# Kernel tuning notes

Measured on AMD Instinct MI355X. Metric: run time of the kernel, lower is better.

The kernel has to match this reference:

```python
import jax, jax.numpy as jnp
import numpy as np

EPS = 1e-5
SLOPE = 0.01  # torch LeakyReLU default negative slope


def _bn(h, gamma, beta):
    # BatchNorm1d in training mode: biased batch statistics over the batch dim
    mu = jnp.mean(h, axis=0)
    var = jnp.var(h, axis=0)
    return gamma * (h - mu) * jax.lax.rsqrt(var + EPS) + beta


def _leaky(h):
    return jnp.where(h >= 0, h, SLOPE * h)


def _forward(x, adj, w_gc1, b_gc1, w_gc2, b_gc2, w_gc3, b_gc3,
             w_fc0, b_fc0, g_fc0, be_fc0, w_fc1, b_fc1, g_fc1, be_fc1, w_fc2, b_fc2):
    B, S, Fp1 = x.shape
    F = Fp1 - 1
    N = adj.shape[0]
    # --- scatter: build per-sample node features from first S-1 timesteps ---
    sids = x[:, :S - 1, -2].astype(jnp.int32)                                   # [B,S-1]
    feats = jnp.concatenate([x[:, :S - 1, :-2], x[:, :S - 1, -1:]], axis=-1)    # [B,S-1,F]
    X = jnp.zeros((B, N, F), x.dtype).at[jnp.arange(B)[:, None], sids].set(feats)
    # --- symmetric-normalized adjacency with self loops: D^-1/2 (A+I) D^-1/2 ---
    A = adj + jnp.eye(N, dtype=adj.dtype)
    d = jax.lax.rsqrt(jnp.sum(A, axis=1))
    Ahat = d[:, None] * A * d[None, :]                                          # [N,N]
    # --- fc0 branch on last-timestep features ---
    h0 = _leaky(_bn(x[:, -1, :-2] @ w_fc0 + b_fc0, g_fc0, be_fc0))              # [B,FH]
    # --- 3-layer GCN: relu(Ahat @ X @ W + b) ---
    X = jax.nn.relu(jnp.einsum('mn,bnf->bmf', Ahat, X) @ w_gc1 + b_gc1)
    X = jax.nn.relu(jnp.einsum('mn,bnf->bmf', Ahat, X) @ w_gc2 + b_gc2)
    X = jax.nn.relu(jnp.einsum('mn,bnf->bmf', Ahat, X) @ w_gc3 + b_gc3)         # [B,N,GH]
    # --- gather station-specific rows ---
    sid_last = x[:, -1, -2].astype(jnp.int32)                                   # [B]
    g = X[jnp.arange(B), sid_last]                                              # [B,GH]
    # --- fusion MLP head ---
    h = jnp.concatenate([h0, g], axis=1)
    h = _leaky(_bn(h @ w_fc1 + b_fc1, g_fc1, be_fc1))
    return jax.nn.sigmoid(h @ w_fc2 + b_fc2)                                    # [B,1]


def setup_inputs() -> dict:
    B, N, S, F = 128, 2000, 64, 16
    GH, FH = 512, 512
    key = jax.random.key(0)
    ks = jax.random.split(key, 12)
    x = jax.random.normal(ks[0], (B, S, F + 1), dtype=jnp.float32)
    # station-id column (-2): unique ids per sample so scatter writes are unambiguous
    perms = jax.vmap(lambda k: jax.random.permutation(k, N)[:S])(jax.random.split(ks[1], B))  # [B,S]
    x = x.at[:, :, -2].set(perms.astype(jnp.float32))
    # random symmetric 0/1 adjacency, avg degree ~32
    adj = (jax.random.uniform(ks[2], (N, N)) < (32.0 / N)).astype(jnp.float32)
    adj = jnp.maximum(adj, adj.T)

    def lin(k, i, o):
        kw, kb = jax.random.split(k)
        bound = 1.0 / np.sqrt(i)
        w = jax.random.uniform(kw, (i, o), jnp.float32, -bound, bound)
        b = jax.random.uniform(kb, (o,), jnp.float32, -bound, bound)
        return w, b

    w_gc1, b_gc1 = lin(ks[3], F, GH // 2)
    w_gc2, b_gc2 = lin(ks[4], GH // 2, GH // 2)
    w_gc3, b_gc3 = lin(ks[5], GH // 2, GH)
    w_fc0, b_fc0 = lin(ks[6], F - 1, FH)
    w_fc1, b_fc1 = lin(ks[7], GH + FH, FH)
    w_fc2, b_fc2 = lin(ks[8], FH, 1)
    g_fc0 = jnp.ones((FH,), jnp.float32)
    be_fc0 = jnp.zeros((FH,), jnp.float32)
    g_fc1 = jnp.ones((FH,), jnp.float32)
    be_fc1 = jnp.zeros((FH,), jnp.float32)
    return dict(x=x, adj=adj, w_gc1=w_gc1, b_gc1=b_gc1, w_gc2=w_gc2, b_gc2=b_gc2,
                w_gc3=w_gc3, b_gc3=b_gc3, w_fc0=w_fc0, b_fc0=b_fc0, g_fc0=g_fc0, be_fc0=be_fc0,
                w_fc1=w_fc1, b_fc1=b_fc1, g_fc1=g_fc1, be_fc1=be_fc1, w_fc2=w_fc2, b_fc2=b_fc2)


def reference(x, adj, w_gc1, b_gc1, w_gc2, b_gc2, w_gc3, b_gc3, w_fc0, b_fc0, g_fc0, be_fc0,
              w_fc1, b_fc1, g_fc1, be_fc1, w_fc2, b_fc2):
    return _forward(x, adj, w_gc1, b_gc1, w_gc2, b_gc2, w_gc3, b_gc3,
                    w_fc0, b_fc0, g_fc0, be_fc0, w_fc1, b_fc1, g_fc1, be_fc1, w_fc2, b_fc2)
```

## Files before the change

kernel.cpp:

```cpp
#include <hip/hip_runtime.h>
#include <hip/hip_bf16.h>

typedef __hip_bfloat16 bf16;
typedef short s8v __attribute__((ext_vector_type(8)));
typedef float f4v __attribute__((ext_vector_type(4)));
typedef float f2v __attribute__((ext_vector_type(2)));

#define B   128
#define N   2000
#define S   64
#define CAP 128
#define JT  16
#define JG  8
#define XROW 1088

__device__ inline ushort bfb(float v) {
    union { __hip_bfloat16 h; ushort u; } c; c.h = __float2bfloat16(v); return c.u;
}

__global__ __launch_bounds__(256) void k_prep0(const float* __restrict__ adj,
                                               float* __restrict__ d,
                                               const float* __restrict__ w1,
                                               const float* __restrict__ w2,
                                               uint4* __restrict__ wf1,
                                               uint4* __restrict__ wf2) {
    int blk = blockIdx.x;
    if (blk < N) {
        int m = blk;
        const float* row = adj + (size_t)m * N;
        float s = 0.f;
        for (int c = threadIdx.x; c < N; c += 256) s += row[c];
        for (int o = 32; o > 0; o >>= 1) s += __shfl_down(s, o);
        __shared__ float red[4];
        int wave = threadIdx.x >> 6;
        if ((threadIdx.x & 63) == 0) red[wave] = s;
        __syncthreads();
        if (threadIdx.x == 0)
            d[m] = rsqrtf(red[0] + red[1] + red[2] + red[3] + 1.0f);
    } else {
        int blk2 = blk - N;
        if (blk2 < 4) {
            int e = blk2 * 256 + threadIdx.x;
            int ct = e >> 6, l = e & 63;
            int kg = l >> 4, ch = ct * 16 + (l & 15);
            ushort h[8];
#pragma unroll
            for (int j = 0; j < 8; ++j) {
                int f = kg * 8 + j;
                h[j] = (f < 16) ? bfb(w1[f * 256 + ch]) : (ushort)0;
            }
            uint4 r;
            r.x = h[0] | ((uint)h[1] << 16);
            r.y = h[2] | ((uint)h[3] << 16);
            r.z = h[4] | ((uint)h[5] << 16);
            r.w = h[6] | ((uint)h[7] << 16);
            wf1[e] = r;
        } else {
            int e = (blk2 - 4) * 256 + threadIdx.x;
            int l = e & 63;
            int kc = (e >> 6) & 7;
            int nt = e >> 9;
            int col = l & 15, kg = l >> 4;
            ushort h[8];
#pragma unroll
            for (int i = 0; i < 8; ++i) {
                int k = kc * 32 + kg * 8 + i;
                h[i] = bfb(w2[k * 256 + nt * 16 + col]);
            }
            uint4 r;
            r.x = h[0] | ((uint)h[1] << 16);
            r.y = h[2] | ((uint)h[3] << 16);
            r.z = h[4] | ((uint)h[5] << 16);
            r.w = h[6] | ((uint)h[7] << 16);
            wf2[e] = r;
        }
    }
}

__global__ __launch_bounds__(256) void k_prep1(const float* __restrict__ adj,
                                               const float* __restrict__ d,
                                               const float* __restrict__ x,
                                               int* __restrict__ cnt,
                                               int* __restrict__ idx,
                                               float* __restrict__ val,
                                               int* __restrict__ sid,
                                               int* __restrict__ sid_last,
                                               uint4* __restrict__ feA,
                                               const float* __restrict__ w0,
                                               const float* __restrict__ b0,
                                               float* __restrict__ hp0,
                                               float* __restrict__ mu0,
                                               float* __restrict__ rstd0) {
    int blk = blockIdx.x;
    if (blk < 500) {
        int m = blk * 4 + (threadIdx.x >> 6);
        int lane = threadIdx.x & 63;
        const float* row = adj + (size_t)m * N;
        float dm = d[m];
        int base = 0;
        for (int c0 = 0; c0 < N; c0 += 64) {
            int c = c0 + lane;
            float a = 0.f;
            if (c < N) { a = row[c]; if (c == m) a += 1.0f; }
            bool pred = (a != 0.f);
            unsigned long long mask = __ballot(pred);
            int pos = base + __popcll(mask & ((1ull << lane) - 1ull));
            if (pred && pos < CAP) {
                idx[m * CAP + pos] = c;
                val[m * CAP + pos] = dm * d[c] * a;
            }
            base += (int)__popcll(mask);
        }
        if (lane == 0) cnt[m] = base < CAP ? base : CAP;
    } else if (blk < 500 + B) {
        int b = blk - 500, tid = threadIdx.x;
        const float* xb = x + (size_t)b * XROW;
        __shared__ float dss_sh[63];
        __shared__ float fe_sh[64][16];
        if (tid < S - 1) {
            int s_ = (int)xb[tid * 17 + 15];
            sid[b * (S - 1) + tid] = s_;
            dss_sh[tid] = d[s_];
        }
        if (tid == S - 1) sid_last[b] = (int)xb[(S - 1) * 17 + 15];
        if (tid >= 240 && tid < 256) fe_sh[63][tid - 240] = 0.f;
        __syncthreads();
        for (int i = tid; i < (S - 1) * 16; i += 256) {
            int t = i >> 4, f = i & 15;
            fe_sh[t][f] = dss_sh[t] * xb[t * 17 + (f < 15 ? f : 16)];
        }
        __syncthreads();
        if (tid < 128) {
            int kc = tid >> 6, l = tid & 63;
            int f = l & 15, tg = l >> 4;
            ushort h[8];
#pragma unroll
            for (int j = 0; j < 8; ++j)
                h[j] = bfb(fe_sh[kc * 32 + tg * 8 + j][f]);
            uint4 r;
            r.x = h[0] | ((uint)h[1] << 16);
            r.y = h[2] | ((uint)h[3] << 16);
            r.z = h[4] | ((uint)h[5] << 16);
            r.w = h[6] | ((uint)h[7] << 16);
            feA[(b * 2 + kc) * 64 + l] = r;
        }
    } else {
        int tid = threadIdx.x;
        int c = tid >> 7, b = tid & 127;
        int o = (blk - 500 - B) * 2 + c;
        const float* xr = x + (size_t)b * XROW + (S - 1) * 17;
        float acc = b0[o];
#pragma unroll
        for (int f = 0; f < 15; ++f) acc += xr[f] * w0[f * 512 + o];
        hp0[b * 512 + o] = acc;
        float s = acc, s2 = acc * acc;
        for (int off = 32; off > 0; off >>= 1) {
            s += __shfl_down(s, off);
            s2 += __shfl_down(s2, off);
        }
        __shared__ float rs[4], rs2[4];
        int wv = tid >> 6;
        if ((tid & 63) == 0) { rs[wv] = s; rs2[wv] = s2; }
        __syncthreads();
        if ((tid & 127) == 0) {
            float S1 = rs[c * 2] + rs[c * 2 + 1];
            float S2 = rs2[c * 2] + rs2[c * 2 + 1];
            float m = S1 * (1.f / B);
            float var = S2 * (1.f / B) - m * m;
            mu0[o] = m;
            rstd0[o] = rsqrtf(var + 1e-5f);
        }
    }
}

__global__ __launch_bounds__(256) void k_x1(const float* __restrict__ adj,
                                            const float* __restrict__ d,
                                            const int* __restrict__ sid,
                                            const uint4* __restrict__ feA,
                                            const uint4* __restrict__ wfrag,
                                            const float* __restrict__ b1,
                                            unsigned char* __restrict__ X1) {
    __shared__ int sv[64];
    __shared__ __align__(16) ushort Ylds[64][40];
    __shared__ float b1s[256];
    __shared__ __align__(16) uint Xs[4][16][68];
    int b = blockIdx.y, p0 = blockIdx.x * 64, tid = threadIdx.x;
    b1s[tid] = b1[tid];
    if (tid < 63) sv[tid] = sid[b * 63 + tid];
    if (tid == 63) sv[63] = 0;
    __syncthreads();

    int l = tid & 63, wv = tid >> 6;
    int lm = l & 15, lg = l >> 4;
    int pt = p0 + wv * 16;
    int pcol = pt + lm;
    bool pv = (pcol < N);
    int pc = pv ? pcol : 0;

    s8v a1_0 = *(const s8v*)&feA[(b * 2 + 0) * 64 + l];
    s8v a1_1 = *(const s8v*)&feA[(b * 2 + 1) * 64 + l];

    int ss[16];
#pragma unroll
    for (int q = 0; q < 16; ++q)
        ss[q] = sv[(q >> 3) * 32 + lg * 8 + (q & 7)];
    float av[16];
#pragma unroll
    for (int q = 0; q < 16; ++q)
        av[q] = adj[(size_t)ss[q] * N + pc];
#pragma unroll
    for (int q = 0; q < 16; ++q) {
        av[q] = pv ? av[q] : 0.f;
        if (pcol == ss[q]) av[q] += 1.0f;
    }
    ushort h[16];
#pragma unroll
    for (int q = 0; q < 16; ++q) h[q] = bfb(av[q]);
    s8v b1f, b2f;
    {
        uint4 t0, t1;
        t0.x = h[0] | ((uint)h[1] << 16);  t0.y = h[2] | ((uint)h[3] << 16);
        t0.z = h[4] | ((uint)h[5] << 16);  t0.w = h[6] | ((uint)h[7] << 16);
        t1.x = h[8] | ((uint)h[9] << 16);  t1.y = h[10] | ((uint)h[11] << 16);
        t1.z = h[12] | ((uint)h[13] << 16); t1.w = h[14] | ((uint)h[15] << 16);
        b1f = *(s8v*)&t0; b2f = *(s8v*)&t1;
    }
    f4v D1 = (f4v){0.f, 0.f, 0.f, 0.f};
    D1 = __builtin_amdgcn_mfma_f32_16x16x32_bf16(a1_0, b1f, D1, 0, 0, 0);
    D1 = __builtin_amdgcn_mfma_f32_16x16x32_bf16(a1_1, b2f, D1, 0, 0, 0);
    float dp = d[pc] * (pv ? 1.f : 0.f);
    uint2 pk;
    pk.x = bfb(D1[0] * dp) | ((uint)bfb(D1[1] * dp) << 16);
    pk.y = bfb(D1[2] * dp) | ((uint)bfb(D1[3] * dp) << 16);
    *(uint2*)&Ylds[wv * 16 + lm][lg * 4] = pk;
    *(uint2*)&Ylds[wv * 16 + lm][16 + lg * 4] = make_uint2(0u, 0u);
    __syncthreads();

    s8v yf = *(const s8v*)&Ylds[wv * 16 + lm][lg * 8];
    f4v acc2[16];
#pragma unroll
    for (int ct = 0; ct < 16; ++ct) acc2[ct] = (f4v){0.f, 0.f, 0.f, 0.f};
#pragma unroll
    for (int ct = 0; ct < 16; ++ct) {
        s8v wfv = *(const s8v*)&wfrag[ct * 64 + l];
        acc2[ct] = __builtin_amdgcn_mfma_f32_16x16x32_bf16(wfv, yf, acc2[ct], 0, 0, 0);
    }
#pragma unroll
    for (int ct = 0; ct < 16; ++ct) {
        float4 bz = *(float4*)&b1s[ct * 16 + lg * 4];
        float v0 = acc2[ct][0] + bz.x; v0 = v0 > 0.f ? v0 : 0.f;
        float v1 = acc2[ct][1] + bz.y; v1 = v1 > 0.f ? v1 : 0.f;
        float v2 = acc2[ct][2] + bz.z; v2 = v2 > 0.f ? v2 : 0.f;
        float v3 = acc2[ct][3] + bz.w; v3 = v3 > 0.f ? v3 : 0.f;
        uint pk8 = (uint)__builtin_amdgcn_cvt_pk_fp8_f32(v0, v1, 0, false);
        pk8 = (uint)__builtin_amdgcn_cvt_pk_fp8_f32(v2, v3, (int)pk8, true);
        Xs[wv][lm][ct * 4 + lg] = pk8;
    }
    __syncthreads();
    {
        uint4* dstb = (uint4*)((uint*)X1 + ((size_t)b * N + p0 + wv * 16) * 64);
#pragma unroll
        for (int i = 0; i < 4; ++i) {
            int g = l + 64 * i;
            int r = g >> 4, c4 = g & 15;
            if (p0 + wv * 16 + r < N)
                dstb[g] = *(uint4*)&Xs[wv][r][c4 * 4];
        }
    }
}

__global__ __launch_bounds__(256) void k_gather(const int* __restrict__ cnt,
                                                const int* __restrict__ idxA,
                                                const float* __restrict__ valA,
                                                const int* __restrict__ sid_last,
                                                const unsigned char* __restrict__ X1,
                                                bf16* __restrict__ aggG) {
    __shared__ int   nns[JG];
    __shared__ int   ncn_s[JG];
    __shared__ int   nidx[JG][CAP];
    __shared__ float nval[JG][CAP];
    int b = blockIdx.y, j0 = blockIdx.x * JG, tid = threadIdx.x;
    int m = sid_last[b];
    int cj = cnt[m];
    if (tid < JG) {
        int j = j0 + tid;
        int n = idxA[m * CAP + (j < cj ? j : 0)];
        nns[tid] = n;
        ncn_s[tid] = (j < cj) ? cnt[n] : 0;
    }
    __syncthreads();
    for (int i = tid; i < JG * CAP; i += 256) {
        int jj = i >> 7, k = i & (CAP - 1);
        int n = nns[jj], c = ncn_s[jj];
        nidx[jj][k] = (k < c) ? idxA[n * CAP + k] : 0;
        nval[jj][k] = (k < c) ? valA[n * CAP + k] : 0.f;
    }
    __syncthreads();
    int lane = tid & 63;
    int w = __builtin_amdgcn_readfirstlane(tid >> 6);
    int la = w * 2, lb = la + 1;
    const uint* X1bl = (const uint*)X1 + (size_t)b * N * 64 + lane;
    int cA = ncn_s[la], cB = ncn_s[lb];
    int cmax = cA > cB ? cA : cB;
    float aA0 = 0.f, aA1 = 0.f, aA2 = 0.f, aA3 = 0.f;
    float aB0 = 0.f, aB1 = 0.f, aB2 = 0.f, aB3 = 0.f;
    if (cmax > 0) {
        uint uA0, uA1, uA2, uA3, uB0, uB1, uB2, uB3;
        float vA0, vA1, vA2, vA3, vB0, vB1, vB2, vB3;
        uA0 = X1bl[(size_t)nidx[la][0] * 64]; vA0 = nval[la][0];
        uA1 = X1bl[(size_t)nidx[la][1] * 64]; vA1 = nval[la][1];
        uA2 = X1bl[(size_t)nidx[la][2] * 64]; vA2 = nval[la][2];
        uA3 = X1bl[(size_t)nidx[la][3] * 64]; vA3 = nval[la][3];
        uB0 = X1bl[(size_t)nidx[lb][0] * 64]; vB0 = nval[lb][0];
        uB1 = X1bl[(size_t)nidx[lb][1] * 64]; vB1 = nval[lb][1];
        uB2 = X1bl[(size_t)nidx[lb][2] * 64]; vB2 = nval[lb][2];
        uB3 = X1bl[(size_t)nidx[lb][3] * 64]; vB3 = nval[lb][3];
        int c4 = (cmax + 3) & ~3;
        for (int k = 0; k < c4; k += 4) {
            uint cA0 = uA0, cA1 = uA1, cA2 = uA2, cA3 = uA3;
            uint cB0 = uB0, cB1 = uB1, cB2 = uB2, cB3 = uB3;
            float wA0 = vA0, wA1 = vA1, wA2 = vA2, wA3 = vA3;
            float wB0 = vB0, wB1 = vB1, wB2 = vB2, wB3 = vB3;
            int k4 = k + 4; k4 = k4 < CAP ? k4 : CAP - 1;
            int k5 = k + 5; k5 = k5 < CAP ? k5 : CAP - 1;
            int k6 = k + 6; k6 = k6 < CAP ? k6 : CAP - 1;
            int k7 = k + 7; k7 = k7 < CAP ? k7 : CAP - 1;
            uA0 = X1bl[(size_t)nidx[la][k4] * 64]; vA0 = nval[la][k4];
            uA1 = X1bl[(size_t)nidx[la][k5] * 64]; vA1 = nval[la][k5];
            uA2 = X1bl[(size_t)nidx[la][k6] * 64]; vA2 = nval[la][k6];
            uA3 = X1bl[(size_t)nidx[la][k7] * 64]; vA3 = nval[la][k7];
            uB0 = X1bl[(size_t)nidx[lb][k4] * 64]; vB0 = nval[lb][k4];
            uB1 = X1bl[(size_t)nidx[lb][k5] * 64]; vB1 = nval[lb][k5];
            uB2 = X1bl[(size_t)nidx[lb][k6] * 64]; vB2 = nval[lb][k6];
            uB3 = X1bl[(size_t)nidx[lb][k7] * 64]; vB3 = nval[lb][k7];
            f2v lo, hi;
            lo = __builtin_amdgcn_cvt_pk_f32_fp8((int)cA0, false);
            hi = __builtin_amdgcn_cvt_pk_f32_fp8((int)cA0, true);
            aA0 += wA0 * lo.x; aA1 += wA0 * lo.y; aA2 += wA0 * hi.x; aA3 += wA0 * hi.y;
            lo = __builtin_amdgcn_cvt_pk_f32_fp8((int)cA1, false);
            hi = __builtin_amdgcn_cvt_pk_f32_fp8((int)cA1, true);
            aA0 += wA1 * lo.x; aA1 += wA1 * lo.y; aA2 += wA1 * hi.x; aA3 += wA1 * hi.y;
            lo = __builtin_amdgcn_cvt_pk_f32_fp8((int)cA2, false);
            hi = __builtin_amdgcn_cvt_pk_f32_fp8((int)cA2, true);
            aA0 += wA2 * lo.x; aA1 += wA2 * lo.y; aA2 += wA2 * hi.x; aA3 += wA2 * hi.y;
            lo = __builtin_amdgcn_cvt_pk_f32_fp8((int)cA3, false);
            hi = __builtin_amdgcn_cvt_pk_f32_fp8((int)cA3, true);
            aA0 += wA3 * lo.x; aA1 += wA3 * lo.y; aA2 += wA3 * hi.x; aA3 += wA3 * hi.y;
            lo = __builtin_amdgcn_cvt_pk_f32_fp8((int)cB0, false);
            hi = __builtin_amdgcn_cvt_pk_f32_fp8((int)cB0, true);
            aB0 += wB0 * lo.x; aB1 += wB0 * lo.y; aB2 += wB0 * hi.x; aB3 += wB0 * hi.y;
            lo = __builtin_amdgcn_cvt_pk_f32_fp8((int)cB1, false);
            hi = __builtin_amdgcn_cvt_pk_f32_fp8((int)cB1, true);
            aB0 += wB1 * lo.x; aB1 += wB1 * lo.y; aB2 += wB1 * hi.x; aB3 += wB1 * hi.y;
            lo = __builtin_amdgcn_cvt_pk_f32_fp8((int)cB2, false);
            hi = __builtin_amdgcn_cvt_pk_f32_fp8((int)cB2, true);
            aB0 += wB2 * lo.x; aB1 += wB2 * lo.y; aB2 += wB2 * hi.x; aB3 += wB2 * hi.y;
            lo = __builtin_amdgcn_cvt_pk_f32_fp8((int)cB3, false);
            hi = __builtin_amdgcn_cvt_pk_f32_fp8((int)cB3, true);
            aB0 += wB3 * lo.x; aB1 += wB3 * lo.y; aB2 += wB3 * hi.x; aB3 += wB3 * hi.y;
        }
    }
    uint2 pkA, pkB;
    pkA.x = bfb(aA0) | ((uint)bfb(aA1) << 16);
    pkA.y = bfb(aA2) | ((uint)bfb(aA3) << 16);
    pkB.x = bfb(aB0) | ((uint)bfb(aB1) << 16);
    pkB.y = bfb(aB2) | ((uint)bfb(aB3) << 16);
    uint2* ag = (uint2*)aggG;
    ag[((size_t)b * CAP + j0 + la) * 64 + lane] = pkA;
    ag[((size_t)b * CAP + j0 + lb) * 64 + lane] = pkB;
}

__global__ __launch_bounds__(256) void k_x2g(const int* __restrict__ cnt,
                                             const int* __restrict__ sid_last,
                                             const float* __restrict__ valA,
                                             const bf16* __restrict__ aggG,
                                             const uint4* __restrict__ w2f,
                                             const float* __restrict__ b2,
                                             float* __restrict__ gaggP) {
    __shared__ ushort agg[JT][264];
    __shared__ float vs[JT];
    int b = blockIdx.y, j0 = blockIdx.x * JT, tid = threadIdx.x;
    int m = sid_last[b];
    int cj = cnt[m];
    if (j0 >= cj) return;
    int nj = cj - j0; if (nj > JT) nj = JT;
    if (tid < JT) vs[tid] = (tid < nj) ? valA[m * CAP + j0 + tid] : 0.f;
    {
        const uint4* src = (const uint4*)(aggG + ((size_t)b * CAP + j0) * 256);
        for (int i = tid; i < 512; i += 256) {
            int row = i >> 5, col = i & 31;
            *(uint4*)&agg[row][col * 8] = src[i];
        }
    }
    __syncthreads();
    int lane = tid & 63;
    int w = __builtin_amdgcn_readfirstlane(tid >> 6);
    int col = lane & 15, rg = lane >> 4;
    s8v af[8];
#pragma unroll
    for (int kc = 0; kc < 8; ++kc)
        af[kc] = *(const s8v*)&agg[col][kc * 32 + rg * 8];
    float* outp = gaggP + ((size_t)b * 8 + blockIdx.x) * 256;
#pragma unroll
    for (int t = 0; t < 4; ++t) {
        int nt = w * 4 + t;
        f4v acc = (f4v){0.f, 0.f, 0.f, 0.f};
#pragma unroll
        for (int kc = 0; kc < 8; ++kc) {
            s8v bf = *(const s8v*)&w2f[(nt * 8 + kc) * 64 + lane];
            acc = __builtin_amdgcn_mfma_f32_16x16x32_bf16(af[kc], bf, acc, 0, 0, 0);
        }
        float bv = b2[nt * 16 + col];
        float p = 0.f;
#pragma unroll
        for (int i = 0; i < 4; ++i) {
            float vv = acc[i] + bv;
            vv = vv > 0.f ? vv : 0.f;
            p += vs[rg * 4 + i] * vv;
        }
        p += __shfl_xor(p, 16);
        p += __shfl_xor(p, 32);
        if (lane < 16) outp[nt * 16 + col] = p;
    }
}

__global__ __launch_bounds__(256) void k_gmm(const int* __restrict__ cnt,
                                             const int* __restrict__ sid_last,
                                             const float* __restrict__ gaggP,
                                             const float* __restrict__ w3,
                                             const float* __restrict__ b3,
                                             float* __restrict__ g) {
    int b = blockIdx.x, ot = blockIdx.y, tid = threadIdx.x;
    __shared__ float h[256];
    {
        int m = sid_last[b];
        int cj = cnt[m];
        int nq = (cj + JT - 1) / JT;
        const float* p = gaggP + (size_t)b * 8 * 256 + tid;
        float s = 0.f;
        for (int q = 0; q < nq; ++q) s += p[q * 256];
        h[tid] = s;
    }
    __syncthreads();
    int q  = tid & 31;
    int kg = tid >> 5;
    const float4* w4 = (const float4*)w3;
    int wq = ot * 32 + q;
    float4 acc = {0.f, 0.f, 0.f, 0.f};
    for (int k = kg * 32; k < kg * 32 + 32; ++k) {
        float hk = h[k];
        float4 w = w4[(size_t)k * 128 + wq];
        acc.x += hk * w.x; acc.y += hk * w.y; acc.z += hk * w.z; acc.w += hk * w.w;
    }
    __shared__ float4 red[8][32];
    red[kg][q] = acc;
    __syncthreads();
    if (tid < 32) {
        float4 s = red[0][tid];
#pragma unroll
        for (int gr = 1; gr < 8; ++gr) {
            float4 r = red[gr][tid];
            s.x += r.x; s.y += r.y; s.z += r.z; s.w += r.w;
        }
        int ob = ot * 128 + tid * 4;
        s.x += b3[ob];     s.x = s.x > 0.f ? s.x : 0.f;
        s.y += b3[ob + 1]; s.y = s.y > 0.f ? s.y : 0.f;
        s.z += b3[ob + 2]; s.z = s.z > 0.f ? s.z : 0.f;
        s.w += b3[ob + 3]; s.w = s.w > 0.f ? s.w : 0.f;
        *(float4*)&g[(size_t)b * 512 + ob] = s;
    }
}

__global__ __launch_bounds__(256) void k_bn1w(const float* __restrict__ h,
                                              float* __restrict__ mu,
                                              float* __restrict__ rstd) {
    int tid = threadIdx.x;
    int o = blockIdx.x * 32 + (tid & 31);
    int bg = tid >> 5;
    float s = 0.f, s2 = 0.f;
    for (int b = bg * 16; b < bg * 16 + 16; ++b) {
        float v = h[b * 512 + o];
        s += v; s2 += v * v;
    }
    __shared__ float rs[8][32], rs2[8][32];
    rs[bg][tid & 31] = s; rs2[bg][tid & 31] = s2;
    __syncthreads();
    if (tid < 32) {
        float S1 = 0.f, S2 = 0.f;
#pragma unroll
        for (int g2 = 0; g2 < 8; ++g2) { S1 += rs[g2][tid]; S2 += rs2[g2][tid]; }
        float m = S1 * (1.f / B);
        float var = S2 * (1.f / B) - m * m;
        mu[blockIdx.x * 32 + tid] = m;
        rstd[blockIdx.x * 32 + tid] = rsqrtf(var + 1e-5f);
    }
}

__global__ __launch_bounds__(256) void k_fc1(const float* __restrict__ hp0,
                                             const float* __restrict__ mu0,
                                             const float* __restrict__ rstd0,
                                             const float* __restrict__ gam,
                                             const float* __restrict__ bet,
                                             const float* __restrict__ gbuf,
                                             const float* __restrict__ w1,
                                             const float* __restrict__ b1,
                                             float* __restrict__ hp1) {
    int b = blockIdx.x, ot = blockIdx.y, tid = threadIdx.x;
    __shared__ float h[1024];
    for (int o = tid; o < 512; o += 256) {
        float v = hp0[b * 512 + o];
        v = gam[o] * (v - mu0[o]) * rstd0[o] + bet[o];
        h[o] = v >= 0.f ? v : 0.01f * v;
        h[512 + o] = gbuf[(size_t)b * 512 + o];
    }
    __syncthreads();
    int q  = tid & 31;
    int kg = tid >> 5;
    const float4* w4 = (const float4*)w1;
    int wq = ot * 32 + q;
    float4 acc = {0.f, 0.f, 0.f, 0.f};
    for (int k = kg * 128; k < kg * 128 + 128; ++k) {
        float hk = h[k];
        float4 w = w4[(size_t)k * 128 + wq];
        acc.x += hk * w.x; acc.y += hk * w.y; acc.z += hk * w.z; acc.w += hk * w.w;
    }
    __shared__ float4 red[8][32];
    red[kg][q] = acc;
    __syncthreads();
    if (tid < 32) {
        float4 s = red[0][tid];
#pragma unroll
        for (int gr = 1; gr < 8; ++gr) {
            float4 r = red[gr][tid];
            s.x += r.x; s.y += r.y; s.z += r.z; s.w += r.w;
        }
        int ob = ot * 128 + tid * 4;
        s.x += b1[ob]; s.y += b1[ob + 1]; s.z += b1[ob + 2]; s.w += b1[ob + 3];
        *(float4*)&hp1[b * 512 + ob] = s;
    }
}

__global__ __launch_bounds__(64) void k_out(const float* __restrict__ hp1,
                                            const float* __restrict__ mu1,
                                            const float* __restrict__ rstd1,
                                            const float* __restrict__ gam,
                                            const float* __restrict__ bet,
                                            const float* __restrict__ w2,
                                            const float* __restrict__ b2,
                                            float* __restrict__ out) {
    int b = blockIdx.x, lane = threadIdx.x;
    float acc = 0.f;
    for (int o = lane; o < 512; o += 64) {
        float v = hp1[b * 512 + o];
        v = gam[o] * (v - mu1[o]) * rstd1[o] + bet[o];
        v = v >= 0.f ? v : 0.01f * v;
        acc += v * w2[o];
    }
    for (int off = 32; off > 0; off >>= 1) acc += __shfl_down(acc, off);
    if (lane == 0) out[b] = 1.f / (1.f + expf(-(acc + b2[0])));
}

static inline size_t align256(size_t x) { return (x + 255) & ~(size_t)255; }

extern "C" void kernel_launch(void* const* d_in, const int* in_sizes, int n_in,
                              void* d_out, int out_size, void* d_ws, size_t ws_size,
                              hipStream_t stream) {
    const float* x     = (const float*)d_in[0];
    const float* adj   = (const float*)d_in[1];
    const float* w_gc1 = (const float*)d_in[2];
    const float* b_gc1 = (const float*)d_in[3];
    const float* w_gc2 = (const float*)d_in[4];
    const float* b_gc2 = (const float*)d_in[5];
    const float* w_gc3 = (const float*)d_in[6];
    const float* b_gc3 = (const float*)d_in[7];
    const float* w_fc0 = (const float*)d_in[8];
    const float* b_fc0 = (const float*)d_in[9];
    const float* g_fc0 = (const float*)d_in[10];
    const float* be_fc0= (const float*)d_in[11];
    const float* w_fc1 = (const float*)d_in[12];
    const float* b_fc1 = (const float*)d_in[13];
    const float* g_fc1 = (const float*)d_in[14];
    const float* be_fc1= (const float*)d_in[15];
    const float* w_fc2 = (const float*)d_in[16];
    const float* b_fc2 = (const float*)d_in[17];

    char* wsp = (char*)d_ws;
    size_t off = 0;
    auto alloc = [&](size_t bytes) { void* p = wsp + off; off = align256(off + bytes); return p; };
    float* d_deg   = (float*)alloc((size_t)N * 4);
    int*   sid     = (int*)  alloc((size_t)B * 63 * 4);
    int*   sidl    = (int*)  alloc((size_t)B * 4);
    uint4* feA     = (uint4*)alloc((size_t)B * 2 * 64 * 16);
    uint4* wfrag   = (uint4*)alloc((size_t)1024 * 16);
    uint4* w2frag  = (uint4*)alloc((size_t)8192 * 16);
    int*   csr_cnt = (int*)  alloc((size_t)N * 4);
    int*   csr_idx = (int*)  alloc((size_t)N * CAP * 4);
    float* csr_val = (float*)alloc((size_t)N * CAP * 4);
    unsigned char* X1 = (unsigned char*)alloc((size_t)B * N * 256);
    bf16*  aggG    = (bf16*) alloc((size_t)B * CAP * 256 * 2);
    float* gaggP   = (float*)alloc((size_t)B * 8 * 256 * 4);
    float* gbuf    = (float*)alloc((size_t)B * 512 * 4);
    float* hp0     = (float*)alloc((size_t)B * 512 * 4);
    float* mu0     = (float*)alloc(512 * 4);
    float* rstd0   = (float*)alloc(512 * 4);
    float* hp1     = (float*)alloc((size_t)B * 512 * 4);
    float* mu1     = (float*)alloc(512 * 4);
    float* rstd1   = (float*)alloc(512 * 4);

    k_prep0 <<<N + 36, 256, 0, stream>>>(adj, d_deg, w_gc1, w_gc2, wfrag, w2frag);
    k_prep1 <<<500 + B + 256, 256, 0, stream>>>(adj, d_deg, x, csr_cnt, csr_idx, csr_val,
                                                sid, sidl, feA, w_fc0, b_fc0, hp0, mu0, rstd0);
    k_x1    <<<dim3(32, B), 256, 0, stream>>>(adj, d_deg, sid, feA, wfrag, b_gc1, X1);
    k_gather<<<dim3(CAP / JG, B), 256, 0, stream>>>(csr_cnt, csr_idx, csr_val, sidl, X1, aggG);
    k_x2g   <<<dim3(CAP / JT, B), 256, 0, stream>>>(csr_cnt, sidl, csr_val, aggG, w2frag, b_gc2, gaggP);
    k_gmm   <<<dim3(B, 4), 256, 0, stream>>>(csr_cnt, sidl, gaggP, w_gc3, b_gc3, gbuf);
    k_fc1   <<<dim3(B, 4), 256, 0, stream>>>(hp0, mu0, rstd0, g_fc0, be_fc0, gbuf, w_fc1, b_fc1, hp1);
    k_bn1w  <<<16, 256, 0, stream>>>(hp1, mu1, rstd1);
    k_out   <<<B, 64, 0, stream>>>(hp1, mu1, rstd1, g_fc1, be_fc1, w_fc2, b_fc2, (float*)d_out);
}
```

Before: 122.7 us.

## Store gathered aggregates as fp8 and alias LDS buffers in k_x1

The intermediate aggregate buffer between k_gather and k_x2g changes from bf16 to fp8, halving its global write and read traffic; k_x2g converts fp8 back to bf16 while staging into LDS. In k_x1 the Ylds and Xs shared arrays are overlaid in a union to cut LDS footprint, at the cost of an extra barrier. The fp8 storage adds quantization error to the layer-2 inputs.

```diff
diff --git a/kernel.cpp b/kernel.cpp
--- a/kernel.cpp
+++ b/kernel.cpp
@@ -181,9 +181,11 @@
                                             const float* __restrict__ b1,
                                             unsigned char* __restrict__ X1) {
     __shared__ int sv[64];
-    __shared__ __align__(16) ushort Ylds[64][40];
     __shared__ float b1s[256];
-    __shared__ __align__(16) uint Xs[4][16][68];
+    __shared__ __align__(16) union SU {
+        ushort Ylds[64][40];
+        uint   Xs[4][16][68];
+    } su;
     int b = blockIdx.y, p0 = blockIdx.x * 64, tid = threadIdx.x;
     b1s[tid] = b1[tid];
     if (tid < 63) sv[tid] = sid[b * 63 + tid];
@@ -232,11 +234,12 @@
     uint2 pk;
     pk.x = bfb(D1[0] * dp) | ((uint)bfb(D1[1] * dp) << 16);
     pk.y = bfb(D1[2] * dp) | ((uint)bfb(D1[3] * dp) << 16);
-    *(uint2*)&Ylds[wv * 16 + lm][lg * 4] = pk;
-    *(uint2*)&Ylds[wv * 16 + lm][16 + lg * 4] = make_uint2(0u, 0u);
-    __syncthreads();
-
-    s8v yf = *(const s8v*)&Ylds[wv * 16 + lm][lg * 8];
+    *(uint2*)&su.Ylds[wv * 16 + lm][lg * 4] = pk;
+    *(uint2*)&su.Ylds[wv * 16 + lm][16 + lg * 4] = make_uint2(0u, 0u);
+    __syncthreads();
+
+    s8v yf = *(const s8v*)&su.Ylds[wv * 16 + lm][lg * 8];
+    __syncthreads();
     f4v acc2[16];
 #pragma unroll
     for (int ct = 0; ct < 16; ++ct) acc2[ct] = (f4v){0.f, 0.f, 0.f, 0.f};
@@ -254,7 +257,7 @@
         float v3 = acc2[ct][3] + bz.w; v3 = v3 > 0.f ? v3 : 0.f;
         uint pk8 = (uint)__builtin_amdgcn_cvt_pk_fp8_f32(v0, v1, 0, false);
         pk8 = (uint)__builtin_amdgcn_cvt_pk_fp8_f32(v2, v3, (int)pk8, true);
-        Xs[wv][lm][ct * 4 + lg] = pk8;
+        su.Xs[wv][lm][ct * 4 + lg] = pk8;
     }
     __syncthreads();
     {
@@ -264,7 +267,7 @@
             int g = l + 64 * i;
             int r = g >> 4, c4 = g & 15;
             if (p0 + wv * 16 + r < N)
-                dstb[g] = *(uint4*)&Xs[wv][r][c4 * 4];
+                dstb[g] = *(uint4*)&su.Xs[wv][r][c4 * 4];
         }
     }
 }
@@ -274,7 +277,7 @@
                                                 const float* __restrict__ valA,
                                                 const int* __restrict__ sid_last,
                                                 const unsigned char* __restrict__ X1,
-                                                bf16* __restrict__ aggG) {
+                                                unsigned char* __restrict__ aggG) {
     __shared__ int   nns[JG];
     __shared__ int   ncn_s[JG];
     __shared__ int   nidx[JG][CAP];
@@ -360,12 +363,11 @@
             aB0 += wB3 * lo.x; aB1 += wB3 * lo.y; aB2 += wB3 * hi.x; aB3 += wB3 * hi.y;
         }
     }
-    uint2 pkA, pkB;
-    pkA.x = bfb(aA0) | ((uint)bfb(aA1) << 16);
-    pkA.y = bfb(aA2) | ((uint)bfb(aA3) << 16);
-    pkB.x = bfb(aB0) | ((uint)bfb(aB1) << 16);
-    pkB.y = bfb(aB2) | ((uint)bfb(aB3) << 16);
-    uint2* ag = (uint2*)aggG;
+    uint pkA = (uint)__builtin_amdgcn_cvt_pk_fp8_f32(aA0, aA1, 0, false);
+    pkA = (uint)__builtin_amdgcn_cvt_pk_fp8_f32(aA2, aA3, (int)pkA, true);
+    uint pkB = (uint)__builtin_amdgcn_cvt_pk_fp8_f32(aB0, aB1, 0, false);
+    pkB = (uint)__builtin_amdgcn_cvt_pk_fp8_f32(aB2, aB3, (int)pkB, true);
+    uint* ag = (uint*)aggG;
     ag[((size_t)b * CAP + j0 + la) * 64 + lane] = pkA;
     ag[((size_t)b * CAP + j0 + lb) * 64 + lane] = pkB;
 }
@@ -373,7 +375,7 @@
 __global__ __launch_bounds__(256) void k_x2g(const int* __restrict__ cnt,
                                              const int* __restrict__ sid_last,
                                              const float* __restrict__ valA,
-                                             const bf16* __restrict__ aggG,
+                                             const unsigned char* __restrict__ aggG,
                                              const uint4* __restrict__ w2f,
                                              const float* __restrict__ b2,
                                              float* __restrict__ gaggP) {
@@ -386,10 +388,16 @@
     int nj = cj - j0; if (nj > JT) nj = JT;
     if (tid < JT) vs[tid] = (tid < nj) ? valA[m * CAP + j0 + tid] : 0.f;
     {
-        const uint4* src = (const uint4*)(aggG + ((size_t)b * CAP + j0) * 256);
-        for (int i = tid; i < 512; i += 256) {
-            int row = i >> 5, col = i & 31;
-            *(uint4*)&agg[row][col * 8] = src[i];
+        const uint* src = (const uint*)aggG + ((size_t)b * CAP + j0) * 64;
+        for (int i = tid; i < JT * 64; i += 256) {
+            int row = i >> 6, ln = i & 63;
+            uint u8 = src[(size_t)row * 64 + ln];
+            f2v lo = __builtin_amdgcn_cvt_pk_f32_fp8((int)u8, false);
+            f2v hi = __builtin_amdgcn_cvt_pk_f32_fp8((int)u8, true);
+            uint2 pk;
+            pk.x = bfb(lo.x) | ((uint)bfb(lo.y) << 16);
+            pk.y = bfb(hi.x) | ((uint)bfb(hi.y) << 16);
+            *(uint2*)&agg[row][ln * 4] = pk;
         }
     }
     __syncthreads();
@@ -596,8 +604,8 @@
     int*   csr_cnt = (int*)  alloc((size_t)N * 4);
     int*   csr_idx = (int*)  alloc((size_t)N * CAP * 4);
     float* csr_val = (float*)alloc((size_t)N * CAP * 4);
-    unsigned char* X1 = (unsigned char*)alloc((size_t)B * N * 256);
-    bf16*  aggG    = (bf16*) alloc((size_t)B * CAP * 256 * 2);
+    unsigned char* X1   = (unsigned char*)alloc((size_t)B * N * 256);
+    unsigned char* aggG = (unsigned char*)alloc((size_t)B * CAP * 256);
     float* gaggP   = (float*)alloc((size_t)B * 8 * 256 * 4);
     float* gbuf    = (float*)alloc((size_t)B * 512 * 4);
     float* hp0     = (float*)alloc((size_t)B * 512 * 4);
```

After: 119.2 us, median of 2. 2.9% less time.
